# Kernel optimization log

Hardware: AMD Instinct MI355X
Metric: run time of the kernel (lower is better)

Reference implementation:

```python
import jax, jax.numpy as jnp
import numpy as np

B = 4          # per_gpu_batch_size
P = 16         # n_contexts
N = B * P      # fused passage dim = 64
L = 512        # seq_len
H = 768        # hidden_size
S = 16         # sentence spans per passage


def setup_inputs() -> dict:
    key = jax.random.key(0)
    k1, k2, k3 = jax.random.split(key, 3)
    hidden_states = jax.random.normal(k1, (N, L, H), jnp.float32)
    # nn.Linear weight [out, in]; original init std=1.0 saturates tanh, use 0.02 scale for sane numerics
    dense_w = jax.random.normal(k2, (H, H), jnp.float32) * 0.02
    dense_b = jnp.zeros((H,), jnp.float32)
    attention_mask = jnp.ones((N, L), jnp.int32)
    # strictly increasing boundaries -> S non-empty, ragged, contiguous spans per passage
    r = jnp.sort(jax.random.randint(k3, (N, S + 1), 0, L - S), axis=-1) + jnp.arange(S + 1, dtype=jnp.int32)
    spans = jnp.stack([r[:, :-1], r[:, 1:]], axis=-1).astype(jnp.int32)  # [N, S, 2]
    return dict(hidden_states=hidden_states, dense_w=dense_w, dense_b=dense_b,
                attention_mask=attention_mask, spans=spans)


def reference(hidden_states, dense_w, dense_b, attention_mask, spans):
    # sentence_spans branch: token_tensor = hidden_states (all tokens)
    # pooled_output = activation(dense(token_tensor)); cls_norm_type == 'none' -> no norm
    pooled = jnp.tanh(jnp.einsum('nlh,oh->nlo', hidden_states, dense_w) + dense_b)  # [N, L, H]
    pooled_output_passages = pooled[:, 0]  # [N, H]
    # ragged per-span mean pooling, vectorized as a masked segment reduce
    pos = jnp.arange(L, dtype=jnp.int32)                         # [L]
    start = spans[..., 0][..., None]                             # [N, S, 1]
    end = spans[..., 1][..., None]                               # [N, S, 1]
    m = ((pos >= start) & (pos < end)).astype(pooled.dtype)      # [N, S, L]
    sums = jnp.einsum('nsl,nlh->nsh', m, pooled)                 # [N, S, H]
    counts = (spans[..., 1] - spans[..., 0]).astype(pooled.dtype)[..., None]  # [N, S, 1]
    sentence_embeddings = (sums / counts).reshape(N * S, H)      # [N*S, H]
    # all S spans valid per passage -> mask of zeros (0 = valid in original code)
    sentence_mask = jnp.zeros((N, S), jnp.float32)
    return pooled_output_passages, sentence_embeddings, sentence_mask
```

## Files before the change

### kernel.cpp

```cpp
#include <hip/hip_runtime.h>
#include <hip/hip_bf16.h>

#define NPASS 64
#define LSEQ  512
#define HDIM  768
#define NSPAN 16
#define MTOT  (NPASS*LSEQ)
#define OFF_SENT (NPASS*HDIM)
#define A_ELEMS (MTOT*HDIM)
#define W_ELEMS (HDIM*HDIM)

#define BM 128
#define BN 128
#define BK 32

typedef __bf16 bf16x8 __attribute__((ext_vector_type(8)));
typedef float  f32x4  __attribute__((ext_vector_type(4)));

__device__ inline unsigned short f2bf(float f) {
  __hip_bfloat16 h = __float2bfloat16(f);
  unsigned short u; __builtin_memcpy(&u, &h, 2); return u;
}

__global__ __launch_bounds__(256) void convert_kernel(
    const float* __restrict__ A, const float* __restrict__ W,
    unsigned short* __restrict__ Ab, unsigned short* __restrict__ Wb)
{
  const long long i = ((long long)blockIdx.x * 256 + threadIdx.x) * 8;
  const float* src; unsigned short* dst; long long off;
  if (i < A_ELEMS) { src = A; dst = Ab; off = i; }
  else             { src = W; dst = Wb; off = i - A_ELEMS; }
  const float4 a = *(const float4*)(src + off);
  const float4 b = *(const float4*)(src + off + 4);
  union { unsigned short us[8]; uint4 v; } o;
  o.us[0]=f2bf(a.x); o.us[1]=f2bf(a.y); o.us[2]=f2bf(a.z); o.us[3]=f2bf(a.w);
  o.us[4]=f2bf(b.x); o.us[5]=f2bf(b.y); o.us[6]=f2bf(b.z); o.us[7]=f2bf(b.w);
  *(uint4*)(dst + off) = o.v;
}

__global__ __launch_bounds__(256) void gemm_fused_kernel(
    const unsigned short* __restrict__ Ab,
    const unsigned short* __restrict__ Wb,
    const float* __restrict__ bias,
    const int* __restrict__ spans,
    float* __restrict__ out)
{
  __shared__ __align__(16) unsigned short As[BM*BK];
  __shared__ __align__(16) unsigned short Bs[BN*BK];
  __shared__ int   sp_st[NSPAN], sp_en[NSPAN];
  __shared__ float inv_s[NSPAN];
  __shared__ short sid_l[BM];
  __shared__ float bias_s[BN];

  const int tid  = threadIdx.x;
  const int wave = tid >> 6;
  const int lane = tid & 63;
  const int quad = lane >> 4;
  const int lr   = lane & 15;
  const int wm   = wave >> 1;
  const int wn   = wave & 1;
  const int tile_n = blockIdx.x * BN;
  const int tile_m = blockIdx.y * BM;
  const int npass  = tile_m >> 9;
  const int l0     = tile_m & 511;

  if (tid < NSPAN) {
    const int st = spans[(npass * NSPAN + tid) * 2 + 0];
    const int en = spans[(npass * NSPAN + tid) * 2 + 1];
    sp_st[tid] = st; sp_en[tid] = en; inv_s[tid] = 1.0f / (float)(en - st);
  }
  if (tid >= 128 && tid < 128 + BN) bias_s[tid - 128] = bias[tile_n + tid - 128];
  __syncthreads();
  if (tid < BM) {
    const int l = l0 + tid;
    short s = -1;
    #pragma unroll
    for (int i = 0; i < NSPAN; ++i)
      if (l >= sp_st[i] && l < sp_en[i]) s = (short)i;
    sid_l[tid] = s;
  }

  const int lrow = lane >> 2;
  const int lcol = (lane & 3) * 8;

  f32x4 acc[4][4];
  #pragma unroll
  for (int i = 0; i < 4; ++i)
    #pragma unroll
    for (int j = 0; j < 4; ++j)
      acc[i][j] = (f32x4){0.f, 0.f, 0.f, 0.f};

  for (int k0 = 0; k0 < HDIM; k0 += BK) {
    #pragma unroll
    for (int j = 0; j < 4; ++j) {
      const int seg = wave * 4 + j;
      if (seg < 8) {
        const unsigned short* g =
            Ab + (size_t)(tile_m + seg * 16 + lrow) * HDIM + (k0 + lcol);
        __builtin_amdgcn_global_load_lds(
            (const __attribute__((address_space(1))) void*)g,
            (__attribute__((address_space(3))) void*)(As + seg * 512),
            16, 0, 0);
      } else {
        const int s2 = seg - 8;
        const unsigned short* g =
            Wb + (size_t)(tile_n + s2 * 16 + lrow) * HDIM + (k0 + lcol);
        __builtin_amdgcn_global_load_lds(
            (const __attribute__((address_space(1))) void*)g,
            (__attribute__((address_space(3))) void*)(Bs + s2 * 512),
            16, 0, 0);
      }
    }
    __syncthreads();

    bf16x8 af[4], bf[4];
    #pragma unroll
    for (int mt = 0; mt < 4; ++mt)
      af[mt] = *(const bf16x8*)(As + ((wm * 64 + mt * 16 + lr) * BK + quad * 8));
    #pragma unroll
    for (int nt = 0; nt < 4; ++nt)
      bf[nt] = *(const bf16x8*)(Bs + ((wn * 64 + nt * 16 + lr) * BK + quad * 8));

    #pragma unroll
    for (int mt = 0; mt < 4; ++mt)
      #pragma unroll
      for (int nt = 0; nt < 4; ++nt)
        acc[mt][nt] = __builtin_amdgcn_mfma_f32_16x16x32_bf16(
            af[mt], bf[nt], acc[mt][nt], 0, 0, 0);

    __syncthreads();
  }

  #pragma unroll
  for (int nt = 0; nt < 4; ++nt) {
    const int lcolo = wn * 64 + nt * 16 + lr;
    const int col   = tile_n + lcolo;
    const float bv  = bias_s[lcolo];
    float* sent_col = out + OFF_SENT + (size_t)(npass * NSPAN) * HDIM + col;
    #pragma unroll
    for (int mt = 0; mt < 4; ++mt) {
      const int rowbase = wm * 64 + mt * 16 + quad * 4;
      int prev = -1; float run = 0.f;
      #pragma unroll
      for (int r = 0; r < 4; ++r) {
        const int lrw = rowbase + r;
        const float v = tanhf(acc[mt][nt][r] + bv);
        if (l0 == 0 && lrw == 0) out[(size_t)npass * HDIM + col] = v;
        const int s = sid_l[lrw];
        if (s != prev) {
          if (prev >= 0) unsafeAtomicAdd(sent_col + (size_t)prev * HDIM, run * inv_s[prev]);
          prev = s; run = 0.f;
        }
        run += v;
      }
      if (prev >= 0) unsafeAtomicAdd(sent_col + (size_t)prev * HDIM, run * inv_s[prev]);
    }
  }
}

extern "C" void kernel_launch(void* const* d_in, const int* in_sizes, int n_in,
                              void* d_out, int out_size, void* d_ws, size_t ws_size,
                              hipStream_t stream) {
  const float* hs  = (const float*)d_in[0];
  const float* w   = (const float*)d_in[1];
  const float* bsc = (const float*)d_in[2];
  const int* spans = (const int*)d_in[4];
  float* out = (float*)d_out;

  unsigned short* Ab = (unsigned short*)d_ws;
  unsigned short* Wb = Ab + A_ELEMS;

  hipMemsetAsync(d_out, 0, (size_t)out_size * sizeof(float), stream);

  convert_kernel<<<dim3((A_ELEMS + W_ELEMS) / 8 / 256), dim3(256), 0, stream>>>(
      hs, w, Ab, Wb);

  dim3 grid(HDIM / BN, MTOT / BM);
  gemm_fused_kernel<<<grid, dim3(256), 0, stream>>>(Ab, Wb, bsc, spans, out);
}
```

Before: 276.5 us.

## Double-buffer GEMM LDS tiles, use fast tanh, and swap grid order

Splits the LDS A/B tiles into two buffers. Each iteration issues the global-to-LDS loads for the next K slice before computing on the current one, so load latency overlaps the MFMA work, and one barrier per iteration is dropped. It also replaces tanhf with an exp/reciprocal approximation, and swaps the grid so M tiles vary fastest along blockIdx.x. The costs are double the LDS footprint, which may lower occupancy, and slightly less accurate tanh.

```diff
diff --git a/kernel.cpp b/kernel.cpp
--- a/kernel.cpp
+++ b/kernel.cpp
@@ -13,6 +13,7 @@
 #define BM 128
 #define BN 128
 #define BK 32
+#define NK (HDIM/BK)
 
 typedef __bf16 bf16x8 __attribute__((ext_vector_type(8)));
 typedef float  f32x4  __attribute__((ext_vector_type(4)));
@@ -20,6 +21,13 @@
 __device__ inline unsigned short f2bf(float f) {
   __hip_bfloat16 h = __float2bfloat16(f);
   unsigned short u; __builtin_memcpy(&u, &h, 2); return u;
+}
+
+__device__ inline float fast_tanh(float x) {
+  const float ax = fabsf(x);
+  const float t  = __expf(-2.0f * ax);
+  const float r  = (1.0f - t) * __builtin_amdgcn_rcpf(1.0f + t);
+  return copysignf(r, x);
 }
 
 __global__ __launch_bounds__(256) void convert_kernel(
@@ -45,8 +53,8 @@
     const int* __restrict__ spans,
     float* __restrict__ out)
 {
-  __shared__ __align__(16) unsigned short As[BM*BK];
-  __shared__ __align__(16) unsigned short Bs[BN*BK];
+  __shared__ __align__(16) unsigned short As[2][BM*BK];
+  __shared__ __align__(16) unsigned short Bs[2][BN*BK];
   __shared__ int   sp_st[NSPAN], sp_en[NSPAN];
   __shared__ float inv_s[NSPAN];
   __shared__ short sid_l[BM];
@@ -59,11 +67,39 @@
   const int lr   = lane & 15;
   const int wm   = wave >> 1;
   const int wn   = wave & 1;
-  const int tile_n = blockIdx.x * BN;
-  const int tile_m = blockIdx.y * BM;
+  const int tile_m = blockIdx.x * BM;
+  const int tile_n = blockIdx.y * BN;
   const int npass  = tile_m >> 9;
   const int l0     = tile_m & 511;
 
+  const int lrow = lane >> 2;
+  const int lcol = (lane & 3) * 8;
+
+  auto stage = [&](int k, int buf) {
+    const int k0 = k * BK;
+    #pragma unroll
+    for (int j = 0; j < 4; ++j) {
+      const int seg = wave * 4 + j;
+      if (seg < 8) {
+        const unsigned short* g =
+            Ab + (size_t)(tile_m + seg * 16 + lrow) * HDIM + (k0 + lcol);
+        __builtin_amdgcn_global_load_lds(
+            (const __attribute__((address_space(1))) void*)g,
+            (__attribute__((address_space(3))) void*)(As[buf] + seg * 512),
+            16, 0, 0);
+      } else {
+        const int s2 = seg - 8;
+        const unsigned short* g =
+            Wb + (size_t)(tile_n + s2 * 16 + lrow) * HDIM + (k0 + lcol);
+        __builtin_amdgcn_global_load_lds(
+            (const __attribute__((address_space(1))) void*)g,
+            (__attribute__((address_space(3))) void*)(Bs[buf] + s2 * 512),
+            16, 0, 0);
+      }
+    }
+  };
+
+  stage(0, 0);
   if (tid < NSPAN) {
     const int st = spans[(npass * NSPAN + tid) * 2 + 0];
     const int en = spans[(npass * NSPAN + tid) * 2 + 1];
@@ -80,9 +116,6 @@
     sid_l[tid] = s;
   }
 
-  const int lrow = lane >> 2;
-  const int lcol = (lane & 3) * 8;
-
   f32x4 acc[4][4];
   #pragma unroll
   for (int i = 0; i < 4; ++i)
@@ -90,36 +123,17 @@
     for (int j = 0; j < 4; ++j)
       acc[i][j] = (f32x4){0.f, 0.f, 0.f, 0.f};
 
-  for (int k0 = 0; k0 < HDIM; k0 += BK) {
-    #pragma unroll
-    for (int j = 0; j < 4; ++j) {
-      const int seg = wave * 4 + j;
-      if (seg < 8) {
-        const unsigned short* g =
-            Ab + (size_t)(tile_m + seg * 16 + lrow) * HDIM + (k0 + lcol);
-        __builtin_amdgcn_global_load_lds(
-            (const __attribute__((address_space(1))) void*)g,
-            (__attribute__((address_space(3))) void*)(As + seg * 512),
-            16, 0, 0);
-      } else {
-        const int s2 = seg - 8;
-        const unsigned short* g =
-            Wb + (size_t)(tile_n + s2 * 16 + lrow) * HDIM + (k0 + lcol);
-        __builtin_amdgcn_global_load_lds(
-            (const __attribute__((address_space(1))) void*)g,
-            (__attribute__((address_space(3))) void*)(Bs + s2 * 512),
-            16, 0, 0);
-      }
-    }
-    __syncthreads();
+  for (int k = 0; k < NK; ++k) {
+    const int cur = k & 1;
+    if (k + 1 < NK) stage(k + 1, cur ^ 1);
 
     bf16x8 af[4], bf[4];
     #pragma unroll
     for (int mt = 0; mt < 4; ++mt)
-      af[mt] = *(const bf16x8*)(As + ((wm * 64 + mt * 16 + lr) * BK + quad * 8));
+      af[mt] = *(const bf16x8*)(As[cur] + ((wm * 64 + mt * 16 + lr) * BK + quad * 8));
     #pragma unroll
     for (int nt = 0; nt < 4; ++nt)
-      bf[nt] = *(const bf16x8*)(Bs + ((wn * 64 + nt * 16 + lr) * BK + quad * 8));
+      bf[nt] = *(const bf16x8*)(Bs[cur] + ((wn * 64 + nt * 16 + lr) * BK + quad * 8));
 
     #pragma unroll
     for (int mt = 0; mt < 4; ++mt)
@@ -144,7 +158,7 @@
       #pragma unroll
       for (int r = 0; r < 4; ++r) {
         const int lrw = rowbase + r;
-        const float v = tanhf(acc[mt][nt][r] + bv);
+        const float v = fast_tanh(acc[mt][nt][r] + bv);
         if (l0 == 0 && lrw == 0) out[(size_t)npass * HDIM + col] = v;
         const int s = sid_l[lrw];
         if (s != prev) {
@@ -175,6 +189,6 @@
   convert_kernel<<<dim3((A_ELEMS + W_ELEMS) / 8 / 256), dim3(256), 0, stream>>>(
       hs, w, Ab, Wb);
 
-  dim3 grid(HDIM / BN, MTOT / BM);
+  dim3 grid(MTOT / BM, HDIM / BN);
   gemm_fused_kernel<<<grid, dim3(256), 0, stream>>>(Ab, Wb, bsc, spans, out);
 }
```

New measurement: 267.4 us. -3.3%, faster.
